# Kernel tuning notes

Measured on AMD Instinct MI355X. Metric: run time of the kernel, lower is better.

## Reference

```python
import jax, jax.numpy as jnp
import numpy as np

BS = 4  # gating blocksize


def setup_inputs() -> dict:
    key = jax.random.key(0)
    k1, k2, k3 = jax.random.split(key, 3)
    batch, rows, width, cols = 8, 2048, 4096, 4096
    X = jax.random.normal(k1, (batch, rows, width), dtype=jnp.float32)
    W = jax.random.normal(k2, (width, cols), dtype=jnp.float32)
    G = jax.random.normal(k3, (batch, width // BS, cols // BS), dtype=jnp.float32)
    return {"X": X, "W": W, "G": G}


def _gmm(X, W, G):
    # Y[b,r,c] = sum_k X[b,r,k] * W[k,c] * G[b, k//BS, c//BS]
    b = X.shape[0]
    # expand block gates to elementwise resolution
    Gf = jnp.repeat(jnp.repeat(G, BS, axis=1), BS, axis=2)  # (b, width, cols)
    # per-batch gated weight, then batched GEMM
    return jnp.einsum('brk,kc,bkc->brc', X, W, Gf)


def reference(X, W, G):
    Y = _gmm(X, W, G)
    s = Y.sum()
    return s * s
```

## Files before the change

kernel.cpp:

```cpp
#include <hip/hip_runtime.h>

#define BATCH 8
#define ROWS  2048
#define WIDTH 4096
#define COLS  4096
#define KB    1024
#define CBV   1024
#define ZPART 32
#define RCH   64
#define NDOT  256

typedef float f32x4 __attribute__((ext_vector_type(4)));

__global__ __launch_bounds__(256) void fused_kernel(const f32x4* __restrict__ X,
                                                    const f32x4* __restrict__ Wv,
                                                    const f32x4* __restrict__ Gv,
                                                    f32x4* __restrict__ part,
                                                    float* __restrict__ wg) {
    const int t = threadIdx.x;
    if (blockIdx.x < 1024) {
        const int s  = blockIdx.x;
        const int k4 = (s & 3) * 256 + t;
        const int b  = (s >> 2) & 7;
        const int z  = s >> 5;

        const f32x4* p = X + (size_t)(b * ROWS + z * RCH) * (WIDTH / 4) + k4;
        f32x4 a = {0.f, 0.f, 0.f, 0.f};
#pragma unroll 8
        for (int r = 0; r < RCH; ++r) {
            f32x4 v = p[(size_t)r * (WIDTH / 4)];
            a.x += v.x; a.y += v.y; a.z += v.z; a.w += v.w;
        }
        part[((size_t)(z * BATCH + b) << 10) + k4] = a;
    } else {
        const int kb = blockIdx.x - 1024;
        const int lane = t & 63, wv = t >> 6;

        f32x4 w[4][4];
#pragma unroll
        for (int j = 0; j < 4; ++j)
#pragma unroll
            for (int m = 0; m < 4; ++m)
                w[j][m] = Wv[(size_t)(4 * kb + j) * CBV + 4 * t + m];

        f32x4 g[8];
#pragma unroll
        for (int b = 0; b < 8; ++b)
            g[b] = Gv[((size_t)(b * KB + kb) << 8) + t];

        float w4[4][4];
#pragma unroll
        for (int j = 0; j < 4; ++j)
#pragma unroll
            for (int m = 0; m < 4; ++m)
                w4[j][m] = (w[j][m].x + w[j][m].y) + (w[j][m].z + w[j][m].w);

        float acc[8][4];
#pragma unroll
        for (int b = 0; b < 8; ++b)
#pragma unroll
            for (int j = 0; j < 4; ++j)
                acc[b][j] = g[b].x * w4[j][0] + g[b].y * w4[j][1] +
                            g[b].z * w4[j][2] + g[b].w * w4[j][3];

        __shared__ float lds[4][32];
#pragma unroll
        for (int v = 0; v < 32; ++v) {
            float x = acc[v >> 2][v & 3];
#pragma unroll
            for (int o = 1; o < 64; o <<= 1) x += __shfl_xor(x, o, 64);
            if (lane == 0) lds[wv][v] = x;
        }
        __syncthreads();
        if (t < 32) {
            float r = (lds[0][t] + lds[1][t]) + (lds[2][t] + lds[3][t]);
            wg[(size_t)(t >> 2) * WIDTH + 4 * kb + (t & 3)] = r;
        }
    }
}

__global__ __launch_bounds__(256) void dot_kernel(const f32x4* __restrict__ part,
                                                  const f32x4* __restrict__ wgv,
                                                  float* __restrict__ partial) {
    const int z  = blockIdx.x >> 3;
    const int kc = blockIdx.x & 7;
    const f32x4* pz = part + ((size_t)z * BATCH << 10);

    float acc = 0.f;
#pragma unroll
    for (int rep = 0; rep < 4; ++rep) {
        const int i = (kc << 10) + rep * 256 + threadIdx.x;
        f32x4 a = pz[i], b = wgv[i];
        acc += a.x * b.x + a.y * b.y + a.z * b.z + a.w * b.w;
    }
#pragma unroll
    for (int o = 1; o < 64; o <<= 1) acc += __shfl_xor(acc, o, 64);
    __shared__ float lds[4];
    const int lane = threadIdx.x & 63, wv = threadIdx.x >> 6;
    if (lane == 0) lds[wv] = acc;
    __syncthreads();
    if (threadIdx.x == 0) partial[blockIdx.x] = (lds[0] + lds[1]) + (lds[2] + lds[3]);
}

__global__ __launch_bounds__(256) void square_kernel(const float* __restrict__ partial,
                                                     float* __restrict__ out) {
    float v = partial[threadIdx.x];
#pragma unroll
    for (int o = 1; o < 64; o <<= 1) v += __shfl_xor(v, o, 64);
    __shared__ float lds[4];
    const int lane = threadIdx.x & 63, wv = threadIdx.x >> 6;
    if (lane == 0) lds[wv] = v;
    __syncthreads();
    if (threadIdx.x == 0) {
        float s = (lds[0] + lds[1]) + (lds[2] + lds[3]);
        out[0] = s * s;
    }
}

extern "C" void kernel_launch(void* const* d_in, const int* in_sizes, int n_in,
                              void* d_out, int out_size, void* d_ws, size_t ws_size,
                              hipStream_t stream) {
    const float* X = (const float*)d_in[0];
    const float* W = (const float*)d_in[1];
    const float* G = (const float*)d_in[2];
    float* out = (float*)d_out;

    float* part    = (float*)d_ws;
    float* wg      = part + (size_t)ZPART * BATCH * WIDTH;
    float* partial = wg + (size_t)BATCH * WIDTH;

    fused_kernel<<<2048, 256, 0, stream>>>((const f32x4*)X, (const f32x4*)W,
                                           (const f32x4*)G, (f32x4*)part, wg);

    dot_kernel<<<NDOT, 256, 0, stream>>>((const f32x4*)part, (const f32x4*)wg, partial);

    square_kernel<<<1, 256, 0, stream>>>(partial, out);
}
```

Before: 83.56 us.

## Fuse X column-sum with gated-weight dot, split wg computation into own kernel

The weight-gate reduction moves into its own kernel that runs first. The X row-chunk column sums are then dotted directly with wg inside the same kernel, with per-block partials written out. This removes the intermediate partial-colsum buffer and the separate dot kernel. The cost is that the X-streaming work no longer overlaps with the wg computation in one launch; it now waits on it serially.

```diff
diff --git a/kernel.cpp b/kernel.cpp
--- a/kernel.cpp
+++ b/kernel.cpp
@@ -6,110 +6,97 @@
 #define COLS  4096
 #define KB    1024
 #define CBV   1024
-#define ZPART 32
 #define RCH   64
-#define NDOT  256
 
 typedef float f32x4 __attribute__((ext_vector_type(4)));
 
-__global__ __launch_bounds__(256) void fused_kernel(const f32x4* __restrict__ X,
-                                                    const f32x4* __restrict__ Wv,
-                                                    const f32x4* __restrict__ Gv,
-                                                    f32x4* __restrict__ part,
-                                                    float* __restrict__ wg) {
-    const int t = threadIdx.x;
-    if (blockIdx.x < 1024) {
-        const int s  = blockIdx.x;
-        const int k4 = (s & 3) * 256 + t;
-        const int b  = (s >> 2) & 7;
-        const int z  = s >> 5;
+__global__ __launch_bounds__(256) void wg_kernel(const f32x4* __restrict__ Wv,
+                                                 const f32x4* __restrict__ Gv,
+                                                 float* __restrict__ wg) {
+    const int t  = threadIdx.x;
+    const int kb = blockIdx.x;
+    const int lane = t & 63, wv = t >> 6;
 
-        const f32x4* p = X + (size_t)(b * ROWS + z * RCH) * (WIDTH / 4) + k4;
-        f32x4 a = {0.f, 0.f, 0.f, 0.f};
-#pragma unroll 8
-        for (int r = 0; r < RCH; ++r) {
-            f32x4 v = p[(size_t)r * (WIDTH / 4)];
-            a.x += v.x; a.y += v.y; a.z += v.z; a.w += v.w;
-        }
-        part[((size_t)(z * BATCH + b) << 10) + k4] = a;
-    } else {
-        const int kb = blockIdx.x - 1024;
-        const int lane = t & 63, wv = t >> 6;
+    f32x4 w[4][4];
+#pragma unroll
+    for (int j = 0; j < 4; ++j)
+#pragma unroll
+        for (int m = 0; m < 4; ++m)
+            w[j][m] = Wv[(size_t)(4 * kb + j) * CBV + 4 * t + m];
 
-        f32x4 w[4][4];
+    f32x4 g[8];
+#pragma unroll
+    for (int b = 0; b < 8; ++b)
+        g[b] = Gv[((size_t)(b * KB + kb) << 8) + t];
+
+    float w4[4][4];
+#pragma unroll
+    for (int j = 0; j < 4; ++j)
+#pragma unroll
+        for (int m = 0; m < 4; ++m)
+            w4[j][m] = (w[j][m].x + w[j][m].y) + (w[j][m].z + w[j][m].w);
+
+    float acc[8][4];
+#pragma unroll
+    for (int b = 0; b < 8; ++b)
 #pragma unroll
         for (int j = 0; j < 4; ++j)
+            acc[b][j] = g[b].x * w4[j][0] + g[b].y * w4[j][1] +
+                        g[b].z * w4[j][2] + g[b].w * w4[j][3];
+
+    __shared__ float lds[4][32];
 #pragma unroll
-            for (int m = 0; m < 4; ++m)
-                w[j][m] = Wv[(size_t)(4 * kb + j) * CBV + 4 * t + m];
-
-        f32x4 g[8];
+    for (int v = 0; v < 32; ++v) {
+        float x = acc[v >> 2][v & 3];
 #pragma unroll
-        for (int b = 0; b < 8; ++b)
-            g[b] = Gv[((size_t)(b * KB + kb) << 8) + t];
-
-        float w4[4][4];
-#pragma unroll
-        for (int j = 0; j < 4; ++j)
-#pragma unroll
-            for (int m = 0; m < 4; ++m)
-                w4[j][m] = (w[j][m].x + w[j][m].y) + (w[j][m].z + w[j][m].w);
-
-        float acc[8][4];
-#pragma unroll
-        for (int b = 0; b < 8; ++b)
-#pragma unroll
-            for (int j = 0; j < 4; ++j)
-                acc[b][j] = g[b].x * w4[j][0] + g[b].y * w4[j][1] +
-                            g[b].z * w4[j][2] + g[b].w * w4[j][3];
-
-        __shared__ float lds[4][32];
-#pragma unroll
-        for (int v = 0; v < 32; ++v) {
-            float x = acc[v >> 2][v & 3];
-#pragma unroll
-            for (int o = 1; o < 64; o <<= 1) x += __shfl_xor(x, o, 64);
-            if (lane == 0) lds[wv][v] = x;
-        }
-        __syncthreads();
-        if (t < 32) {
-            float r = (lds[0][t] + lds[1][t]) + (lds[2][t] + lds[3][t]);
-            wg[(size_t)(t >> 2) * WIDTH + 4 * kb + (t & 3)] = r;
-        }
+        for (int o = 1; o < 64; o <<= 1) x += __shfl_xor(x, o, 64);
+        if (lane == 0) lds[wv][v] = x;
+    }
+    __syncthreads();
+    if (t < 32) {
+        float r = (lds[0][t] + lds[1][t]) + (lds[2][t] + lds[3][t]);
+        wg[(size_t)(t >> 2) * WIDTH + 4 * kb + (t & 3)] = r;
     }
 }
 
-__global__ __launch_bounds__(256) void dot_kernel(const f32x4* __restrict__ part,
-                                                  const f32x4* __restrict__ wgv,
-                                                  float* __restrict__ partial) {
-    const int z  = blockIdx.x >> 3;
-    const int kc = blockIdx.x & 7;
-    const f32x4* pz = part + ((size_t)z * BATCH << 10);
+__global__ __launch_bounds__(256) void colsum_dot_kernel(const f32x4* __restrict__ X,
+                                                         const f32x4* __restrict__ wg4,
+                                                         float* __restrict__ partial) {
+    const int t  = threadIdx.x;
+    const int s  = blockIdx.x;
+    const int k4 = (s & 3) * 256 + t;
+    const int b  = (s >> 2) & 7;
+    const int z  = s >> 5;
 
-    float acc = 0.f;
+    const f32x4* p = X + (size_t)(b * ROWS + z * RCH) * (WIDTH / 4) + k4;
+    f32x4 a = {0.f, 0.f, 0.f, 0.f};
+#pragma unroll 8
+    for (int r = 0; r < RCH; ++r) {
+        f32x4 v = p[(size_t)r * (WIDTH / 4)];
+        a.x += v.x; a.y += v.y; a.z += v.z; a.w += v.w;
+    }
+
+    f32x4 wv = wg4[((size_t)b << 10) + k4];
+    float d = a.x * wv.x + a.y * wv.y + a.z * wv.z + a.w * wv.w;
+
 #pragma unroll
-    for (int rep = 0; rep < 4; ++rep) {
-        const int i = (kc << 10) + rep * 256 + threadIdx.x;
-        f32x4 a = pz[i], b = wgv[i];
-        acc += a.x * b.x + a.y * b.y + a.z * b.z + a.w * b.w;
-    }
+    for (int o = 1; o < 64; o <<= 1) d += __shfl_xor(d, o, 64);
+    __shared__ float lds[4];
+    const int lane = t & 63, wvi = t >> 6;
+    if (lane == 0) lds[wvi] = d;
+    __syncthreads();
+    if (t == 0) partial[s] = (lds[0] + lds[1]) + (lds[2] + lds[3]);
+}
+
+__global__ __launch_bounds__(256) void square_kernel(const f32x4* __restrict__ partial4,
+                                                     float* __restrict__ out) {
+    f32x4 v = partial4[threadIdx.x];
+    float acc = (v.x + v.y) + (v.z + v.w);
 #pragma unroll
     for (int o = 1; o < 64; o <<= 1) acc += __shfl_xor(acc, o, 64);
     __shared__ float lds[4];
     const int lane = threadIdx.x & 63, wv = threadIdx.x >> 6;
     if (lane == 0) lds[wv] = acc;
-    __syncthreads();
-    if (threadIdx.x == 0) partial[blockIdx.x] = (lds[0] + lds[1]) + (lds[2] + lds[3]);
-}
-
-__global__ __launch_bounds__(256) void square_kernel(const float* __restrict__ partial,
-                                                     float* __restrict__ out) {
-    float v = partial[threadIdx.x];
-#pragma unroll
-    for (int o = 1; o < 64; o <<= 1) v += __shfl_xor(v, o, 64);
-    __shared__ float lds[4];
-    const int lane = threadIdx.x & 63, wv = threadIdx.x >> 6;
-    if (lane == 0) lds[wv] = v;
     __syncthreads();
     if (threadIdx.x == 0) {
         float s = (lds[0] + lds[1]) + (lds[2] + lds[3]);
@@ -125,14 +112,12 @@
     const float* G = (const float*)d_in[2];
     float* out = (float*)d_out;
 
-    float* part    = (float*)d_ws;
-    float* wg      = part + (size_t)ZPART * BATCH * WIDTH;
+    float* wg      = (float*)d_ws;
     float* partial = wg + (size_t)BATCH * WIDTH;
 
-    fused_kernel<<<2048, 256, 0, stream>>>((const f32x4*)X, (const f32x4*)W,
-                                           (const f32x4*)G, (f32x4*)part, wg);
+    wg_kernel<<<KB, 256, 0, stream>>>((const f32x4*)W, (const f32x4*)G, wg);
 
-    dot_kernel<<<NDOT, 256, 0, stream>>>((const f32x4*)part, (const f32x4*)wg, partial);
+    colsum_dot_kernel<<<1024, 256, 0, stream>>>((const f32x4*)X, (const f32x4*)wg, partial);
 
-    square_kernel<<<1, 256, 0, stream>>>(partial, out);
+    square_kernel<<<1, 256, 0, stream>>>((const f32x4*)partial, out);
 }
```

New measurement: 80.43 us. -3.7%, faster.
